# Kernel optimization log

Measured on AMD Instinct MI355X. Metric: run time of the kernel, lower is better.

## Reference

```python
import jax, jax.numpy as jnp
import numpy as np

NBITS = 3      # weight LSQ bits
PBITS = 8      # partial-sum LSQ bits
EPS = 1e-5


def round_ste(x):
    # straight-through round: identity gradient
    return x + jax.lax.stop_gradient(jnp.round(x) - x)


def lsq(x, alpha, nbits):
    # learned-step-size quantize/dequantize (symmetric signed)
    qn = -(2 ** (nbits - 1))
    qp = 2 ** (nbits - 1) - 1
    return round_ste(jnp.clip(x / alpha, qn, qp)) * alpha


def split_views(x):
    # x: [B,C,H,W] -> 9 shifted views of the 1-padded input, stacked [9,B,C,H,W]
    B, C, H, W = x.shape
    xp = jnp.pad(x, ((0, 0), (0, 0), (1, 1), (1, 1)))
    views = [xp[:, :, di:di + H, dj:dj + W] for dj in range(3) for di in range(3)]
    return jnp.stack(views, 0)


def split_conv3x3(x, w, wa, pa):
    # 3x3 conv emulated as 9 shifted 1x1 LSQ convs with quantized partial-sum accumulate
    # w: [9,O,C] per-tap 1x1 weights, wa: [9] weight step sizes, pa: [9] psum step sizes
    xs = split_views(x)                                      # [9,B,C,H,W]
    wq = jax.vmap(lambda wk, ak: lsq(wk, ak, NBITS))(w, wa)  # [9,O,C]
    ps = jnp.einsum('kbchw,koc->kbohw', xs, wq)              # 9 partial sums
    psq = lsq(ps, pa[:, None, None, None, None], PBITS)      # PartialSumLSQ each tap
    return psq.sum(0)                                        # accumulate -> [B,O,H,W]


def batchnorm(x, g, b):
    m = x.mean((0, 2, 3), keepdims=True)
    v = x.var((0, 2, 3), keepdims=True)
    return (x - m) / jnp.sqrt(v + EPS) * g[None, :, None, None] + b[None, :, None, None]


def setup_inputs() -> dict:
    key = jax.random.key(0)
    ks = jax.random.split(key, 8)
    B, C, O, H, W = 16, 128, 128, 56, 56
    x = jax.random.normal(ks[0], (B, C, H, W), jnp.float32)
    w1 = jax.random.normal(ks[1], (9, O, C), jnp.float32) * 0.05
    w2 = jax.random.normal(ks[2], (9, O, O), jnp.float32) * 0.05
    qp_w = 2 ** (NBITS - 1) - 1
    wa1 = 2.0 * jnp.mean(jnp.abs(w1), axis=(1, 2)) / np.sqrt(qp_w)
    wa2 = 2.0 * jnp.mean(jnp.abs(w2), axis=(1, 2)) / np.sqrt(qp_w)
    pa1 = jnp.full((9,), 0.05, jnp.float32)
    pa2 = jnp.full((9,), 0.05, jnp.float32)
    g1 = jnp.ones((O,), jnp.float32); b1 = jnp.zeros((O,), jnp.float32)
    g2 = jnp.ones((O,), jnp.float32); b2 = jnp.zeros((O,), jnp.float32)
    return {'x': x, 'w1': w1, 'wa1': wa1, 'pa1': pa1, 'g1': g1, 'b1': b1,
            'w2': w2, 'wa2': wa2, 'pa2': pa2, 'g2': g2, 'b2': b2}


def reference(x, w1, wa1, pa1, g1, b1, w2, wa2, pa2, g2, b2):
    identity = x
    out = split_conv3x3(x, w1, wa1, pa1)
    out = jax.nn.relu(batchnorm(out, g1, b1))
    out = split_conv3x3(out, w2, wa2, pa2)
    out = batchnorm(out, g2, b2)
    return jax.nn.relu(out + identity)
```

## Files before the change

kernel.cpp:

```cpp
#include <hip/hip_runtime.h>
#include <math.h>

typedef _Float16 f16;
typedef _Float16 half8 __attribute__((ext_vector_type(8)));
typedef float floatx16 __attribute__((ext_vector_type(16)));
typedef unsigned int u32;

#define HW_     3136
#define NPC     50176.0f
#define PB      3364
#define PPLANE  53824
#define ASTRIDE (2 * PPLANE * 16)

#define SW(c, px) (((px) + ((c) >> 2) + ((c) & 3) * 8) & 63)

typedef __attribute__((address_space(3))) u32 lds_u32;
typedef __attribute__((address_space(1))) u32 glb_u32;
__device__ __forceinline__ void async_copy16(const void* g, void* l) {
    __builtin_amdgcn_global_load_lds((const glb_u32*)g, (lds_u32*)l, 16, 0, 0);
}

__global__ __launch_bounds__(256) void prep_kernel(
        const float* __restrict__ w1, const float* __restrict__ wa1,
        const float* __restrict__ w2, const float* __restrict__ wa2,
        f16* __restrict__ W2a, f16* __restrict__ W2b) {
    const int idx = blockIdx.x * 256 + threadIdx.x;
    const float* w;
    const float* wa;
    f16* o;
    int m;
    if (idx < 18432) { w = w1; wa = wa1; o = W2a; m = idx; }
    else             { w = w2; wa = wa2; o = W2b; m = idx - 18432; }
    const int tap = m >> 11;
    const int r = m & 2047;
    const int k2 = r >> 7;
    const int oc = r & 127;
    const float a = wa[tap];
    const float* src = w + ((size_t)(tap * 128 + oc) * 128 + k2 * 8);
    half8 hv;
#pragma unroll
    for (int j = 0; j < 8; ++j)
        hv[j] = (f16)rintf(fminf(fmaxf(src[j] / a, -4.f), 3.f));
    *(half8*)(o + (size_t)m * 8) = hv;
}

__global__ __launch_bounds__(256) void pad_kernel(char* __restrict__ X2) {
    const int idx = blockIdx.x * 256 + threadIdx.x;
    const int k2 = idx / 3648;
    const int r = idx - k2 * 3648;
    const int b = r / 228;
    const int j = r - b * 228;
    int h, w;
    if (j < 58)        { h = 0;  w = j; }
    else if (j < 116)  { h = 57; w = j - 58; }
    else { const int k = j - 116; h = 1 + (k >> 1); w = (k & 1) * 57; }
    const size_t chunk = (size_t)k2 * PPLANE + (size_t)b * PB + h * 58 + w;
    float4 z = {0.f, 0.f, 0.f, 0.f};
    *(float4*)(X2 + chunk * 16) = z;
}

__global__ __launch_bounds__(256) void pack_kernel(
        const float* __restrict__ x, char* __restrict__ X2,
        float* __restrict__ stats) {
    const int t = threadIdx.x;
    const int blk = blockIdx.x;
    if (blk == 0 && t < 512) stats[t] = 0.f;
    const int b = blk / 49;
    const int p0 = (blk - b * 49) * 64;
    const int px = t & 63;
    const int cq = t >> 6;
    const int p = p0 + px;
    const int h = p / 56;
    const int w = p - h * 56;
    const size_t pp = (size_t)b * PB + (h + 1) * 58 + (w + 1);
    const float* xb = x + (size_t)b * 128 * HW_ + p;
#pragma unroll
    for (int s = 0; s < 4; ++s) {
        const int cg = s * 4 + cq;
        half8 hv, lv;
#pragma unroll
        for (int j = 0; j < 8; ++j) {
            const float v = xb[(size_t)(cg * 8 + j) * HW_];
            const f16 hh = (f16)v;
            hv[j] = hh;
            lv[j] = (f16)(v - (float)hh);
        }
        *(half8*)(X2 + ((size_t)cg * PPLANE + pp) * 16) = hv;
        *(half8*)(X2 + ((size_t)(cg + 16) * PPLANE + pp) * 16) = lv;
    }
}

__global__ __launch_bounds__(256, 2) void conv_kernel(
        const char* __restrict__ X2, const char* __restrict__ W2,
        const float* __restrict__ wav, const float* __restrict__ pav,
        float* __restrict__ cbuf, float* __restrict__ stats) {
    __shared__ f16 Bls[2][16384];
    __shared__ float red[512];
    const int t = threadIdx.x;
    const int lane = t & 63;
    const int wv = t >> 6;
    const int wm = wv & 1, wn = wv >> 1;
    const int tile = (blockIdx.x & 7) * 49 + (blockIdx.x >> 3);
    const int kh = lane >> 5;
    const int ln = lane & 31;

    int ppad[2];
#pragma unroll
    for (int mt = 0; mt < 2; ++mt) {
        const int gp = tile * 128 + wm * 64 + mt * 32 + ln;
        const int b = gp / HW_;
        const int p = gp - b * HW_;
        const int h = p / 56;
        const int w = p - h * 56;
        ppad[mt] = b * PB + (h + 1) * 58 + (w + 1);
    }
    int bdsoff[2];
#pragma unroll
    for (int nt = 0; nt < 2; ++nt)
        bdsoff[nt] = (kh * 128 + wn * 64 + nt * 32 + ln) * 16;
    const int sbase = wv * 8;

    floatx16 facc[2][2];
#pragma unroll
    for (int mt = 0; mt < 2; ++mt)
#pragma unroll
        for (int nt = 0; nt < 2; ++nt)
#pragma unroll
            for (int r = 0; r < 16; ++r) facc[mt][nt][r] = 0.f;

#pragma unroll
    for (int i = 0; i < 8; ++i)
        async_copy16(W2 + (((sbase + i) * 64 + lane) << 4),
                     (void*)&Bls[0][(sbase + i) * 512]);
    int aoff[2], aoffn[2];
#pragma unroll
    for (int mt = 0; mt < 2; ++mt) {
        aoff[mt] = ((ppad[mt] - 59) + kh * PPLANE) << 4;
        aoffn[mt] = aoff[mt];
    }
    half8 afr[2][8];
#pragma unroll
    for (int s0 = 0; s0 < 8; ++s0)
#pragma unroll
        for (int mt = 0; mt < 2; ++mt)
            afr[mt][s0] = *(const half8*)(X2 + aoff[mt] + s0 * ASTRIDE);
    __syncthreads();

    for (int tap = 0; tap < 9; ++tap) {
        const float pak = pav[tap];
        const float s1 = wav[tap] / pak;
        const char* bcur = (const char*)&Bls[tap & 1][0];
        if (tap < 8) {
            const char* wt = W2 + (tap + 1) * 32768;
            f16* bnxt = &Bls[(tap + 1) & 1][0];
#pragma unroll
            for (int i = 0; i < 8; ++i)
                async_copy16(wt + (((sbase + i) * 64 + lane) << 4),
                             (void*)&bnxt[(sbase + i) * 512]);
            const int dn = ((tap + 1) % 3 - 1) * 58 + ((tap + 1) / 3 - 1);
#pragma unroll
            for (int mt = 0; mt < 2; ++mt)
                aoffn[mt] = ((ppad[mt] + dn) + kh * PPLANE) << 4;
        }
        half8 bds[2][2];
#pragma unroll
        for (int nt = 0; nt < 2; ++nt)
#pragma unroll
            for (int sl = 0; sl < 2; ++sl)
                bds[nt][sl] = *(const half8*)(bcur + sl * 4096 + bdsoff[nt]);

        floatx16 acc[2][2];
#pragma unroll
        for (int mt = 0; mt < 2; ++mt)
#pragma unroll
            for (int nt = 0; nt < 2; ++nt)
#pragma unroll
                for (int r = 0; r < 16; ++r) acc[mt][nt][r] = 0.f;

#pragma unroll
        for (int s = 0; s < 16; ++s) {
#pragma unroll
            for (int nt = 0; nt < 2; ++nt)
#pragma unroll
                for (int mt = 0; mt < 2; ++mt)
                    acc[mt][nt] = __builtin_amdgcn_mfma_f32_32x32x16_f16(
                        afr[mt][s & 7], bds[nt][s & 1], acc[mt][nt], 0, 0, 0);
            if (s <= 13) {
                const int kf2 = (s + 2) & 7;
#pragma unroll
                for (int nt = 0; nt < 2; ++nt)
                    bds[nt][s & 1] =
                        *(const half8*)(bcur + kf2 * 4096 + bdsoff[nt]);
            }
            if (s < 8) {
#pragma unroll
                for (int mt = 0; mt < 2; ++mt)
                    afr[mt][s & 7] =
                        *(const half8*)(X2 + aoff[mt] + (s + 8) * ASTRIDE);
            } else if (tap < 8) {
#pragma unroll
                for (int mt = 0; mt < 2; ++mt)
                    afr[mt][s & 7] =
                        *(const half8*)(X2 + aoffn[mt] + (s - 8) * ASTRIDE);
            }
        }

#pragma unroll
        for (int mt = 0; mt < 2; ++mt)
#pragma unroll
            for (int nt = 0; nt < 2; ++nt)
#pragma unroll
                for (int r = 0; r < 16; ++r) {
                    const float q =
                        rintf(fminf(fmaxf(acc[mt][nt][r] * s1, -128.f), 127.f));
                    facc[mt][nt][r] = fmaf(q, pak, facc[mt][nt][r]);
                }
        aoff[0] = aoffn[0];
        aoff[1] = aoffn[1];
        __syncthreads();
    }

    const int gpb = tile * 128 + wm * 64;
    const int ocb = wn * 64 + ln;
#pragma unroll
    for (int mt = 0; mt < 2; ++mt)
#pragma unroll
        for (int r = 0; r < 16; ++r) {
            const int row = (r & 3) + 8 * (r >> 2) + 4 * kh;
            const int gp = gpb + mt * 32 + row;
            float* rp = cbuf + (size_t)gp * 128 + ocb;
            rp[0]  = facc[mt][0][r];
            rp[32] = facc[mt][1][r];
        }

    float sv[2], qv[2];
#pragma unroll
    for (int nt = 0; nt < 2; ++nt) {
        float s = 0.f, q = 0.f;
#pragma unroll
        for (int mt = 0; mt < 2; ++mt)
#pragma unroll
            for (int r = 0; r < 16; ++r) {
                const float v = facc[mt][nt][r];
                s += v;
                q = fmaf(v, v, q);
            }
        s += __shfl_xor(s, 32, 64);
        q += __shfl_xor(q, 32, 64);
        sv[nt] = s; qv[nt] = q;
    }
    if (lane < 32) {
#pragma unroll
        for (int nt = 0; nt < 2; ++nt) {
            const int oc = wn * 64 + nt * 32 + lane;
            red[oc * 2 + wm] = sv[nt];
            red[256 + oc * 2 + wm] = qv[nt];
        }
    }
    __syncthreads();
    if (t < 128) {
        atomicAdd(&stats[t],       red[2 * t] + red[2 * t + 1]);
        atomicAdd(&stats[128 + t], red[256 + 2 * t] + red[256 + 2 * t + 1]);
    }
}

__global__ __launch_bounds__(256) void bn_split_kernel(
        const float* __restrict__ cbuf, const float* __restrict__ stats,
        const float* __restrict__ g, const float* __restrict__ bb,
        char* __restrict__ X2) {
    __shared__ float xs[8192];
    __shared__ float scs[128], shs[128];
    const int t = threadIdx.x;
    if (t < 128) {
        const float m = stats[t] * (1.f / NPC);
        const float var = stats[128 + t] * (1.f / NPC) - m * m;
        const float inv = 1.f / sqrtf(var + 1e-5f);
        const float sc = g[t] * inv;
        scs[t] = sc;
        shs[t] = bb[t] - m * sc;
    }
    __syncthreads();
    const int blk = blockIdx.x;
#pragma unroll
    for (int i = 0; i < 8; ++i) {
        const int idx = i * 256 + t;
        const int px = idx >> 5;
        const int q = idx & 31;
        const float4 v = *(const float4*)&cbuf[(size_t)(blk * 64 + px) * 128 + q * 4];
        const float vv[4] = {v.x, v.y, v.z, v.w};
#pragma unroll
        for (int j = 0; j < 4; ++j) {
            const int c = q * 4 + j;
            xs[c * 64 + SW(c, px)] = fmaxf(fmaf(vv[j], scs[c], shs[c]), 0.f);
        }
    }
    __syncthreads();
    const int b = blk / 49;
    const int p0 = (blk - b * 49) * 64;
    const int px = t & 63;
    const int cq = t >> 6;
    const int p = p0 + px;
    const int h = p / 56;
    const int w = p - h * 56;
    const size_t pp = (size_t)b * PB + (h + 1) * 58 + (w + 1);
#pragma unroll
    for (int s = 0; s < 4; ++s) {
        const int cg = s * 4 + cq;
        half8 hv, lv;
#pragma unroll
        for (int j = 0; j < 8; ++j) {
            const int c = cg * 8 + j;
            const float v = xs[c * 64 + SW(c, px)];
            const f16 hh = (f16)v;
            hv[j] = hh;
            lv[j] = (f16)(v - (float)hh);
        }
        *(half8*)(X2 + ((size_t)cg * PPLANE + pp) * 16) = hv;
        *(half8*)(X2 + ((size_t)(cg + 16) * PPLANE + pp) * 16) = lv;
    }
}

__global__ __launch_bounds__(256) void final_kernel(
        const float* __restrict__ cbuf, const float* __restrict__ stats,
        const float* __restrict__ g, const float* __restrict__ bb,
        const float* __restrict__ resid, float* __restrict__ out) {
    __shared__ float xs[8192];
    __shared__ float scs[128], shs[128];
    const int t = threadIdx.x;
    if (t < 128) {
        const float m = stats[t] * (1.f / NPC);
        const float var = stats[128 + t] * (1.f / NPC) - m * m;
        const float inv = 1.f / sqrtf(var + 1e-5f);
        const float sc = g[t] * inv;
        scs[t] = sc;
        shs[t] = bb[t] - m * sc;
    }
    __syncthreads();
    const int blk = blockIdx.x;
#pragma unroll
    for (int i = 0; i < 8; ++i) {
        const int idx = i * 256 + t;
        const int px = idx >> 5;
        const int q = idx & 31;
        const float4 v = *(const float4*)&cbuf[(size_t)(blk * 64 + px) * 128 + q * 4];
        const float vv[4] = {v.x, v.y, v.z, v.w};
#pragma unroll
        for (int j = 0; j < 4; ++j) {
            const int c = q * 4 + j;
            xs[c * 64 + SW(c, px)] = fmaf(vv[j], scs[c], shs[c]);
        }
    }
    __syncthreads();
    const int b = blk / 49;
    const int p0 = (blk - b * 49) * 64;
    const int lane = t & 63, wq = t >> 6;
#pragma unroll
    for (int i = 0; i < 32; ++i) {
        const int c = i * 4 + wq;
        const float v = xs[c * 64 + SW(c, lane)];
        const size_t gi = (size_t)(b * 128 + c) * HW_ + p0 + lane;
        out[gi] = fmaxf(v + resid[gi], 0.f);
    }
}

extern "C" void kernel_launch(void* const* d_in, const int* in_sizes, int n_in,
                              void* d_out, int out_size, void* d_ws, size_t ws_size,
                              hipStream_t stream) {
    const float* x   = (const float*)d_in[0];
    const float* w1  = (const float*)d_in[1];
    const float* wa1 = (const float*)d_in[2];
    const float* pa1 = (const float*)d_in[3];
    const float* g1  = (const float*)d_in[4];
    const float* b1  = (const float*)d_in[5];
    const float* w2  = (const float*)d_in[6];
    const float* wa2 = (const float*)d_in[7];
    const float* pa2 = (const float*)d_in[8];
    const float* g2  = (const float*)d_in[9];
    const float* b2  = (const float*)d_in[10];
    float* out = (float*)d_out;

    char* ws = (char*)d_ws;
    char*  X2    = ws;
    float* cbuf  = (float*)(ws + 27557888);
    f16*   W2a   = (f16*)(ws + 53248000);
    f16*   W2b   = (f16*)(ws + 53542912);
    float* stats = (float*)(ws + 53837824);
    float* stats1 = stats;
    float* stats2 = stats + 256;

    hipLaunchKernelGGL(prep_kernel, dim3(144), dim3(256), 0, stream,
                       w1, wa1, w2, wa2, W2a, W2b);
    hipLaunchKernelGGL(pad_kernel, dim3(456), dim3(256), 0, stream, X2);
    hipLaunchKernelGGL(pack_kernel, dim3(784), dim3(256), 0, stream,
                       x, X2, stats);
    hipLaunchKernelGGL(conv_kernel, dim3(392), dim3(256), 0, stream,
                       X2, (const char*)W2a, wa1, pa1, cbuf, stats1);
    hipLaunchKernelGGL(bn_split_kernel, dim3(784), dim3(256), 0, stream,
                       cbuf, stats1, g1, b1, X2);
    hipLaunchKernelGGL(conv_kernel, dim3(392), dim3(256), 0, stream,
                       X2, (const char*)W2b, wa2, pa2, cbuf, stats2);
    hipLaunchKernelGGL(final_kernel, dim3(784), dim3(256), 0, stream,
                       cbuf, stats2, g2, b2, x, out);
}
```

Measured before the change: 211.0 us.

## Split conv tiles by output-channel half, drop LDS weight staging, fuse setup kernels

Result: slower. 380.6 us (+80.4%).

```diff
diff --git a/kernel.cpp b/kernel.cpp
--- a/kernel.cpp
+++ b/kernel.cpp
@@ -14,49 +14,43 @@
 
 #define SW(c, px) (((px) + ((c) >> 2) + ((c) & 3) * 8) & 63)
 
-typedef __attribute__((address_space(3))) u32 lds_u32;
-typedef __attribute__((address_space(1))) u32 glb_u32;
-__device__ __forceinline__ void async_copy16(const void* g, void* l) {
-    __builtin_amdgcn_global_load_lds((const glb_u32*)g, (lds_u32*)l, 16, 0, 0);
-}
-
-__global__ __launch_bounds__(256) void prep_kernel(
+__global__ __launch_bounds__(256) void setup_kernel(
         const float* __restrict__ w1, const float* __restrict__ wa1,
         const float* __restrict__ w2, const float* __restrict__ wa2,
-        f16* __restrict__ W2a, f16* __restrict__ W2b) {
+        f16* __restrict__ W2a, f16* __restrict__ W2b, char* __restrict__ X2) {
     const int idx = blockIdx.x * 256 + threadIdx.x;
-    const float* w;
-    const float* wa;
-    f16* o;
-    int m;
-    if (idx < 18432) { w = w1; wa = wa1; o = W2a; m = idx; }
-    else             { w = w2; wa = wa2; o = W2b; m = idx - 18432; }
-    const int tap = m >> 11;
-    const int r = m & 2047;
-    const int k2 = r >> 7;
-    const int oc = r & 127;
-    const float a = wa[tap];
-    const float* src = w + ((size_t)(tap * 128 + oc) * 128 + k2 * 8);
-    half8 hv;
-#pragma unroll
-    for (int j = 0; j < 8; ++j)
-        hv[j] = (f16)rintf(fminf(fmaxf(src[j] / a, -4.f), 3.f));
-    *(half8*)(o + (size_t)m * 8) = hv;
-}
-
-__global__ __launch_bounds__(256) void pad_kernel(char* __restrict__ X2) {
-    const int idx = blockIdx.x * 256 + threadIdx.x;
-    const int k2 = idx / 3648;
-    const int r = idx - k2 * 3648;
-    const int b = r / 228;
-    const int j = r - b * 228;
-    int h, w;
-    if (j < 58)        { h = 0;  w = j; }
-    else if (j < 116)  { h = 57; w = j - 58; }
-    else { const int k = j - 116; h = 1 + (k >> 1); w = (k & 1) * 57; }
-    const size_t chunk = (size_t)k2 * PPLANE + (size_t)b * PB + h * 58 + w;
-    float4 z = {0.f, 0.f, 0.f, 0.f};
-    *(float4*)(X2 + chunk * 16) = z;
+    if (idx < 36864) {
+        const float* w;
+        const float* wa;
+        f16* o;
+        int m;
+        if (idx < 18432) { w = w1; wa = wa1; o = W2a; m = idx; }
+        else             { w = w2; wa = wa2; o = W2b; m = idx - 18432; }
+        const int tap = m >> 11;
+        const int r = m & 2047;
+        const int k2 = r >> 7;
+        const int oc = r & 127;
+        const float a = wa[tap];
+        const float* src = w + ((size_t)(tap * 128 + oc) * 128 + k2 * 8);
+        half8 hv;
+#pragma unroll
+        for (int j = 0; j < 8; ++j)
+            hv[j] = (f16)rintf(fminf(fmaxf(src[j] / a, -4.f), 3.f));
+        *(half8*)(o + (size_t)m * 8) = hv;
+    } else {
+        const int m = idx - 36864;
+        const int k2 = m / 3648;
+        const int r = m - k2 * 3648;
+        const int b = r / 228;
+        const int j = r - b * 228;
+        int h, w;
+        if (j < 58)        { h = 0;  w = j; }
+        else if (j < 116)  { h = 57; w = j - 58; }
+        else { const int k = j - 116; h = 1 + (k >> 1); w = (k & 1) * 57; }
+        const size_t chunk = (size_t)k2 * PPLANE + (size_t)b * PB + h * 58 + w;
+        float4 z = {0.f, 0.f, 0.f, 0.f};
+        *(float4*)(X2 + chunk * 16) = z;
+    }
 }
 
 __global__ __launch_bounds__(256) void pack_kernel(
@@ -90,177 +84,123 @@
     }
 }
 
-__global__ __launch_bounds__(256, 2) void conv_kernel(
+__global__ __launch_bounds__(256, 3) void conv_kernel(
         const char* __restrict__ X2, const char* __restrict__ W2,
         const float* __restrict__ wav, const float* __restrict__ pav,
         float* __restrict__ cbuf, float* __restrict__ stats) {
-    __shared__ f16 Bls[2][16384];
-    __shared__ float red[512];
+    __shared__ float red[256];
     const int t = threadIdx.x;
     const int lane = t & 63;
     const int wv = t >> 6;
     const int wm = wv & 1, wn = wv >> 1;
-    const int tile = (blockIdx.x & 7) * 49 + (blockIdx.x >> 3);
-    const int kh = lane >> 5;
-    const int ln = lane & 31;
-
-    int ppad[2];
+    const int blk = (blockIdx.x & 7) * 98 + (blockIdx.x >> 3);
+    const int pxt = blk >> 1;
+    const int oh = blk & 1;
+    const int kh = lane >> 5, ln = lane & 31;
+    const int ocb = oh * 64 + wn * 32;
+    const int bv = (kh * 128 + ocb + ln) << 4;
+
+    int aoff[2];
 #pragma unroll
     for (int mt = 0; mt < 2; ++mt) {
-        const int gp = tile * 128 + wm * 64 + mt * 32 + ln;
+        const int gp = pxt * 128 + wm * 64 + mt * 32 + ln;
         const int b = gp / HW_;
         const int p = gp - b * HW_;
         const int h = p / 56;
         const int w = p - h * 56;
-        ppad[mt] = b * PB + (h + 1) * 58 + (w + 1);
-    }
-    int bdsoff[2];
-#pragma unroll
-    for (int nt = 0; nt < 2; ++nt)
-        bdsoff[nt] = (kh * 128 + wn * 64 + nt * 32 + ln) * 16;
-    const int sbase = wv * 8;
-
-    floatx16 facc[2][2];
+        aoff[mt] = ((b * PB + (h + 1) * 58 + (w + 1) - 59) + kh * PPLANE) << 4;
+    }
+
+    half8 bfr[8];
+#pragma unroll
+    for (int kf = 0; kf < 8; ++kf)
+        bfr[kf] = *(const half8*)(W2 + bv + kf * 4096);
+    half8 afr[2][4];
+#pragma unroll
+    for (int c = 0; c < 4; ++c)
+#pragma unroll
+        for (int mt = 0; mt < 2; ++mt)
+            afr[mt][c] = *(const half8*)(X2 + aoff[mt] + c * ASTRIDE);
+
+    floatx16 facc[2];
 #pragma unroll
     for (int mt = 0; mt < 2; ++mt)
 #pragma unroll
-        for (int nt = 0; nt < 2; ++nt)
-#pragma unroll
-            for (int r = 0; r < 16; ++r) facc[mt][nt][r] = 0.f;
-
-#pragma unroll
-    for (int i = 0; i < 8; ++i)
-        async_copy16(W2 + (((sbase + i) * 64 + lane) << 4),
-                     (void*)&Bls[0][(sbase + i) * 512]);
-    int aoff[2], aoffn[2];
-#pragma unroll
-    for (int mt = 0; mt < 2; ++mt) {
-        aoff[mt] = ((ppad[mt] - 59) + kh * PPLANE) << 4;
-        aoffn[mt] = aoff[mt];
-    }
-    half8 afr[2][8];
-#pragma unroll
-    for (int s0 = 0; s0 < 8; ++s0)
-#pragma unroll
-        for (int mt = 0; mt < 2; ++mt)
-            afr[mt][s0] = *(const half8*)(X2 + aoff[mt] + s0 * ASTRIDE);
-    __syncthreads();
+        for (int r = 0; r < 16; ++r) facc[mt][r] = 0.f;
 
     for (int tap = 0; tap < 9; ++tap) {
         const float pak = pav[tap];
         const float s1 = wav[tap] / pak;
-        const char* bcur = (const char*)&Bls[tap & 1][0];
-        if (tap < 8) {
-            const char* wt = W2 + (tap + 1) * 32768;
-            f16* bnxt = &Bls[(tap + 1) & 1][0];
-#pragma unroll
-            for (int i = 0; i < 8; ++i)
-                async_copy16(wt + (((sbase + i) * 64 + lane) << 4),
-                             (void*)&bnxt[(sbase + i) * 512]);
-            const int dn = ((tap + 1) % 3 - 1) * 58 + ((tap + 1) / 3 - 1);
-#pragma unroll
-            for (int mt = 0; mt < 2; ++mt)
-                aoffn[mt] = ((ppad[mt] + dn) + kh * PPLANE) << 4;
-        }
-        half8 bds[2][2];
-#pragma unroll
-        for (int nt = 0; nt < 2; ++nt)
-#pragma unroll
-            for (int sl = 0; sl < 2; ++sl)
-                bds[nt][sl] = *(const half8*)(bcur + sl * 4096 + bdsoff[nt]);
-
-        floatx16 acc[2][2];
+        const int dd = (((tap == 2) | (tap == 5)) ? -115 : 58) << 4;
+        const int aoffn0 = aoff[0] + dd;
+        const int aoffn1 = aoff[1] + dd;
+        const char* wnxt = W2 + (tap + 1) * 32768 + bv;
+
+        floatx16 acc[2];
 #pragma unroll
         for (int mt = 0; mt < 2; ++mt)
 #pragma unroll
-            for (int nt = 0; nt < 2; ++nt)
-#pragma unroll
-                for (int r = 0; r < 16; ++r) acc[mt][nt][r] = 0.f;
+            for (int r = 0; r < 16; ++r) acc[mt][r] = 0.f;
 
 #pragma unroll
         for (int s = 0; s < 16; ++s) {
-#pragma unroll
-            for (int nt = 0; nt < 2; ++nt)
-#pragma unroll
-                for (int mt = 0; mt < 2; ++mt)
-                    acc[mt][nt] = __builtin_amdgcn_mfma_f32_32x32x16_f16(
-                        afr[mt][s & 7], bds[nt][s & 1], acc[mt][nt], 0, 0, 0);
-            if (s <= 13) {
-                const int kf2 = (s + 2) & 7;
-#pragma unroll
-                for (int nt = 0; nt < 2; ++nt)
-                    bds[nt][s & 1] =
-                        *(const half8*)(bcur + kf2 * 4096 + bdsoff[nt]);
+            acc[0] = __builtin_amdgcn_mfma_f32_32x32x16_f16(
+                afr[0][s & 3], bfr[s & 7], acc[0], 0, 0, 0);
+            acc[1] = __builtin_amdgcn_mfma_f32_32x32x16_f16(
+                afr[1][s & 3], bfr[s & 7], acc[1], 0, 0, 0);
+            if (s < 12) {
+                afr[0][s & 3] = *(const half8*)(X2 + aoff[0] + (s + 4) * ASTRIDE);
+                afr[1][s & 3] = *(const half8*)(X2 + aoff[1] + (s + 4) * ASTRIDE);
+            } else if (tap < 8) {
+                afr[0][s & 3] = *(const half8*)(X2 + aoffn0 + (s - 12) * ASTRIDE);
+                afr[1][s & 3] = *(const half8*)(X2 + aoffn1 + (s - 12) * ASTRIDE);
             }
-            if (s < 8) {
-#pragma unroll
-                for (int mt = 0; mt < 2; ++mt)
-                    afr[mt][s & 7] =
-                        *(const half8*)(X2 + aoff[mt] + (s + 8) * ASTRIDE);
-            } else if (tap < 8) {
-#pragma unroll
-                for (int mt = 0; mt < 2; ++mt)
-                    afr[mt][s & 7] =
-                        *(const half8*)(X2 + aoffn[mt] + (s - 8) * ASTRIDE);
+            if (tap < 8 && s >= 8)
+                bfr[s - 8] = *(const half8*)(wnxt + (s - 8) * 4096);
+        }
+
+#pragma unroll
+        for (int mt = 0; mt < 2; ++mt)
+#pragma unroll
+            for (int r = 0; r < 16; ++r) {
+                const float q = rintf(
+                    __builtin_amdgcn_fmed3f(acc[mt][r] * s1, -128.f, 127.f));
+                facc[mt][r] = fmaf(q, pak, facc[mt][r]);
             }
-        }
-
-#pragma unroll
-        for (int mt = 0; mt < 2; ++mt)
-#pragma unroll
-            for (int nt = 0; nt < 2; ++nt)
-#pragma unroll
-                for (int r = 0; r < 16; ++r) {
-                    const float q =
-                        rintf(fminf(fmaxf(acc[mt][nt][r] * s1, -128.f), 127.f));
-                    facc[mt][nt][r] = fmaf(q, pak, facc[mt][nt][r]);
-                }
-        aoff[0] = aoffn[0];
-        aoff[1] = aoffn[1];
-        __syncthreads();
-    }
-
-    const int gpb = tile * 128 + wm * 64;
-    const int ocb = wn * 64 + ln;
+        aoff[0] = aoffn0;
+        aoff[1] = aoffn1;
+    }
+
+    const int gpb = pxt * 128 + wm * 64;
 #pragma unroll
     for (int mt = 0; mt < 2; ++mt)
 #pragma unroll
         for (int r = 0; r < 16; ++r) {
             const int row = (r & 3) + 8 * (r >> 2) + 4 * kh;
-            const int gp = gpb + mt * 32 + row;
-            float* rp = cbuf + (size_t)gp * 128 + ocb;
-            rp[0]  = facc[mt][0][r];
-            rp[32] = facc[mt][1][r];
-        }
-
-    float sv[2], qv[2];
-#pragma unroll
-    for (int nt = 0; nt < 2; ++nt) {
-        float s = 0.f, q = 0.f;
-#pragma unroll
-        for (int mt = 0; mt < 2; ++mt)
-#pragma unroll
-            for (int r = 0; r < 16; ++r) {
-                const float v = facc[mt][nt][r];
-                s += v;
-                q = fmaf(v, v, q);
-            }
-        s += __shfl_xor(s, 32, 64);
-        q += __shfl_xor(q, 32, 64);
-        sv[nt] = s; qv[nt] = q;
-    }
+            cbuf[(size_t)(gpb + mt * 32 + row) * 128 + ocb + ln] = facc[mt][r];
+        }
+
+    float s = 0.f, q = 0.f;
+#pragma unroll
+    for (int mt = 0; mt < 2; ++mt)
+#pragma unroll
+        for (int r = 0; r < 16; ++r) {
+            const float v = facc[mt][r];
+            s += v;
+            q = fmaf(v, v, q);
+        }
+    s += __shfl_xor(s, 32, 64);
+    q += __shfl_xor(q, 32, 64);
     if (lane < 32) {
-#pragma unroll
-        for (int nt = 0; nt < 2; ++nt) {
-            const int oc = wn * 64 + nt * 32 + lane;
-            red[oc * 2 + wm] = sv[nt];
-            red[256 + oc * 2 + wm] = qv[nt];
-        }
-    }
-    __syncthreads();
-    if (t < 128) {
-        atomicAdd(&stats[t],       red[2 * t] + red[2 * t + 1]);
-        atomicAdd(&stats[128 + t], red[256 + 2 * t] + red[256 + 2 * t + 1]);
+        const int ol = wn * 32 + lane;
+        red[ol * 2 + wm] = s;
+        red[128 + ol * 2 + wm] = q;
+    }
+    __syncthreads();
+    if (t < 64) {
+        atomicAdd(&stats[oh * 64 + t], red[2 * t] + red[2 * t + 1]);
+        atomicAdd(&stats[128 + oh * 64 + t],
+                  red[128 + 2 * t] + red[128 + 2 * t + 1]);
     }
 }
 
@@ -388,16 +328,15 @@
     float* stats1 = stats;
     float* stats2 = stats + 256;
 
-    hipLaunchKernelGGL(prep_kernel, dim3(144), dim3(256), 0, stream,
-                       w1, wa1, w2, wa2, W2a, W2b);
-    hipLaunchKernelGGL(pad_kernel, dim3(456), dim3(256), 0, stream, X2);
+    hipLaunchKernelGGL(setup_kernel, dim3(600), dim3(256), 0, stream,
+                       w1, wa1, w2, wa2, W2a, W2b, X2);
     hipLaunchKernelGGL(pack_kernel, dim3(784), dim3(256), 0, stream,
                        x, X2, stats);
-    hipLaunchKernelGGL(conv_kernel, dim3(392), dim3(256), 0, stream,
+    hipLaunchKernelGGL(conv_kernel, dim3(784), dim3(256), 0, stream,
                        X2, (const char*)W2a, wa1, pa1, cbuf, stats1);
     hipLaunchKernelGGL(bn_split_kernel, dim3(784), dim3(256), 0, stream,
                        cbuf, stats1, g1, b1, X2);
-    hipLaunchKernelGGL(conv_kernel, dim3(392), dim3(256), 0, stream,
+    hipLaunchKernelGGL(conv_kernel, dim3(784), dim3(256), 0, stream,
                        X2, (const char*)W2b, wa2, pa2, cbuf, stats2);
     hipLaunchKernelGGL(final_kernel, dim3(784), dim3(256), 0, stream,
                        cbuf, stats2, g2, b2, x, out);
```

## Halve conv pixel tile to 64, double grid, merge prep and pad kernels

Applied to the files above, without the earlier changes.

New measurement: 224.1 us. 1.06x slower.

```diff
diff --git a/kernel.cpp b/kernel.cpp
--- a/kernel.cpp
+++ b/kernel.cpp
@@ -20,43 +20,43 @@
     __builtin_amdgcn_global_load_lds((const glb_u32*)g, (lds_u32*)l, 16, 0, 0);
 }
 
-__global__ __launch_bounds__(256) void prep_kernel(
+__global__ __launch_bounds__(256) void setup_kernel(
         const float* __restrict__ w1, const float* __restrict__ wa1,
         const float* __restrict__ w2, const float* __restrict__ wa2,
-        f16* __restrict__ W2a, f16* __restrict__ W2b) {
+        f16* __restrict__ W2a, f16* __restrict__ W2b, char* __restrict__ X2) {
     const int idx = blockIdx.x * 256 + threadIdx.x;
-    const float* w;
-    const float* wa;
-    f16* o;
-    int m;
-    if (idx < 18432) { w = w1; wa = wa1; o = W2a; m = idx; }
-    else             { w = w2; wa = wa2; o = W2b; m = idx - 18432; }
-    const int tap = m >> 11;
-    const int r = m & 2047;
-    const int k2 = r >> 7;
-    const int oc = r & 127;
-    const float a = wa[tap];
-    const float* src = w + ((size_t)(tap * 128 + oc) * 128 + k2 * 8);
-    half8 hv;
-#pragma unroll
-    for (int j = 0; j < 8; ++j)
-        hv[j] = (f16)rintf(fminf(fmaxf(src[j] / a, -4.f), 3.f));
-    *(half8*)(o + (size_t)m * 8) = hv;
-}
-
-__global__ __launch_bounds__(256) void pad_kernel(char* __restrict__ X2) {
-    const int idx = blockIdx.x * 256 + threadIdx.x;
-    const int k2 = idx / 3648;
-    const int r = idx - k2 * 3648;
-    const int b = r / 228;
-    const int j = r - b * 228;
-    int h, w;
-    if (j < 58)        { h = 0;  w = j; }
-    else if (j < 116)  { h = 57; w = j - 58; }
-    else { const int k = j - 116; h = 1 + (k >> 1); w = (k & 1) * 57; }
-    const size_t chunk = (size_t)k2 * PPLANE + (size_t)b * PB + h * 58 + w;
-    float4 z = {0.f, 0.f, 0.f, 0.f};
-    *(float4*)(X2 + chunk * 16) = z;
+    if (idx < 36864) {
+        const float* w;
+        const float* wa;
+        f16* o;
+        int m;
+        if (idx < 18432) { w = w1; wa = wa1; o = W2a; m = idx; }
+        else             { w = w2; wa = wa2; o = W2b; m = idx - 18432; }
+        const int tap = m >> 11;
+        const int r = m & 2047;
+        const int k2 = r >> 7;
+        const int oc = r & 127;
+        const float a = wa[tap];
+        const float* src = w + ((size_t)(tap * 128 + oc) * 128 + k2 * 8);
+        half8 hv;
+#pragma unroll
+        for (int j = 0; j < 8; ++j)
+            hv[j] = (f16)rintf(fminf(fmaxf(src[j] / a, -4.f), 3.f));
+        *(half8*)(o + (size_t)m * 8) = hv;
+    } else {
+        const int m = idx - 36864;
+        const int k2 = m / 3648;
+        const int r = m - k2 * 3648;
+        const int b = r / 228;
+        const int j = r - b * 228;
+        int h, w;
+        if (j < 58)        { h = 0;  w = j; }
+        else if (j < 116)  { h = 57; w = j - 58; }
+        else { const int k = j - 116; h = 1 + (k >> 1); w = (k & 1) * 57; }
+        const size_t chunk = (size_t)k2 * PPLANE + (size_t)b * PB + h * 58 + w;
+        float4 z = {0.f, 0.f, 0.f, 0.f};
+        *(float4*)(X2 + chunk * 16) = z;
+    }
 }
 
 __global__ __launch_bounds__(256) void pack_kernel(
@@ -100,50 +100,39 @@
     const int lane = t & 63;
     const int wv = t >> 6;
     const int wm = wv & 1, wn = wv >> 1;
-    const int tile = (blockIdx.x & 7) * 49 + (blockIdx.x >> 3);
+    const int tile = (blockIdx.x & 7) * 98 + (blockIdx.x >> 3);
     const int kh = lane >> 5;
     const int ln = lane & 31;
 
-    int ppad[2];
-#pragma unroll
-    for (int mt = 0; mt < 2; ++mt) {
-        const int gp = tile * 128 + wm * 64 + mt * 32 + ln;
-        const int b = gp / HW_;
-        const int p = gp - b * HW_;
-        const int h = p / 56;
-        const int w = p - h * 56;
-        ppad[mt] = b * PB + (h + 1) * 58 + (w + 1);
-    }
+    const int gp = tile * 64 + wm * 32 + ln;
+    const int b = gp / HW_;
+    const int p = gp - b * HW_;
+    const int h = p / 56;
+    const int w = p - h * 56;
+    const int ppad = b * PB + (h + 1) * 58 + (w + 1);
+
     int bdsoff[2];
 #pragma unroll
     for (int nt = 0; nt < 2; ++nt)
         bdsoff[nt] = (kh * 128 + wn * 64 + nt * 32 + ln) * 16;
     const int sbase = wv * 8;
 
-    floatx16 facc[2][2];
-#pragma unroll
-    for (int mt = 0; mt < 2; ++mt)
-#pragma unroll
-        for (int nt = 0; nt < 2; ++nt)
-#pragma unroll
-            for (int r = 0; r < 16; ++r) facc[mt][nt][r] = 0.f;
+    floatx16 facc[2];
+#pragma unroll
+    for (int nt = 0; nt < 2; ++nt)
+#pragma unroll
+        for (int r = 0; r < 16; ++r) facc[nt][r] = 0.f;
 
 #pragma unroll
     for (int i = 0; i < 8; ++i)
         async_copy16(W2 + (((sbase + i) * 64 + lane) << 4),
                      (void*)&Bls[0][(sbase + i) * 512]);
-    int aoff[2], aoffn[2];
-#pragma unroll
-    for (int mt = 0; mt < 2; ++mt) {
-        aoff[mt] = ((ppad[mt] - 59) + kh * PPLANE) << 4;
-        aoffn[mt] = aoff[mt];
-    }
-    half8 afr[2][8];
+    int aoff = ((ppad - 59) + kh * PPLANE) << 4;
+    int aoffn = aoff;
+    half8 afr[8];
 #pragma unroll
     for (int s0 = 0; s0 < 8; ++s0)
-#pragma unroll
-        for (int mt = 0; mt < 2; ++mt)
-            afr[mt][s0] = *(const half8*)(X2 + aoff[mt] + s0 * ASTRIDE);
+        afr[s0] = *(const half8*)(X2 + aoff + s0 * ASTRIDE);
     __syncthreads();
 
     for (int tap = 0; tap < 9; ++tap) {
@@ -158,93 +147,72 @@
                 async_copy16(wt + (((sbase + i) * 64 + lane) << 4),
                              (void*)&bnxt[(sbase + i) * 512]);
             const int dn = ((tap + 1) % 3 - 1) * 58 + ((tap + 1) / 3 - 1);
-#pragma unroll
-            for (int mt = 0; mt < 2; ++mt)
-                aoffn[mt] = ((ppad[mt] + dn) + kh * PPLANE) << 4;
-        }
-        half8 bds[2][2];
+            aoffn = ((ppad + dn) + kh * PPLANE) << 4;
+        }
+        half8 bds[2][4];
 #pragma unroll
         for (int nt = 0; nt < 2; ++nt)
 #pragma unroll
-            for (int sl = 0; sl < 2; ++sl)
+            for (int sl = 0; sl < 4; ++sl)
                 bds[nt][sl] = *(const half8*)(bcur + sl * 4096 + bdsoff[nt]);
 
-        floatx16 acc[2][2];
-#pragma unroll
-        for (int mt = 0; mt < 2; ++mt)
-#pragma unroll
-            for (int nt = 0; nt < 2; ++nt)
-#pragma unroll
-                for (int r = 0; r < 16; ++r) acc[mt][nt][r] = 0.f;
+        floatx16 acc[2];
+#pragma unroll
+        for (int nt = 0; nt < 2; ++nt)
+#pragma unroll
+            for (int r = 0; r < 16; ++r) acc[nt][r] = 0.f;
 
 #pragma unroll
         for (int s = 0; s < 16; ++s) {
-#pragma unroll
-            for (int nt = 0; nt < 2; ++nt)
-#pragma unroll
-                for (int mt = 0; mt < 2; ++mt)
-                    acc[mt][nt] = __builtin_amdgcn_mfma_f32_32x32x16_f16(
-                        afr[mt][s & 7], bds[nt][s & 1], acc[mt][nt], 0, 0, 0);
-            if (s <= 13) {
-                const int kf2 = (s + 2) & 7;
+            acc[0] = __builtin_amdgcn_mfma_f32_32x32x16_f16(
+                afr[s & 7], bds[0][s & 3], acc[0], 0, 0, 0);
+            acc[1] = __builtin_amdgcn_mfma_f32_32x32x16_f16(
+                afr[s & 7], bds[1][s & 3], acc[1], 0, 0, 0);
+            if (s <= 11) {
+                const int kf4 = (s + 4) & 7;
 #pragma unroll
                 for (int nt = 0; nt < 2; ++nt)
-                    bds[nt][s & 1] =
-                        *(const half8*)(bcur + kf2 * 4096 + bdsoff[nt]);
+                    bds[nt][s & 3] =
+                        *(const half8*)(bcur + kf4 * 4096 + bdsoff[nt]);
             }
             if (s < 8) {
-#pragma unroll
-                for (int mt = 0; mt < 2; ++mt)
-                    afr[mt][s & 7] =
-                        *(const half8*)(X2 + aoff[mt] + (s + 8) * ASTRIDE);
+                afr[s & 7] = *(const half8*)(X2 + aoff + (s + 8) * ASTRIDE);
             } else if (tap < 8) {
-#pragma unroll
-                for (int mt = 0; mt < 2; ++mt)
-                    afr[mt][s & 7] =
-                        *(const half8*)(X2 + aoffn[mt] + (s - 8) * ASTRIDE);
+                afr[s & 7] = *(const half8*)(X2 + aoffn + (s - 8) * ASTRIDE);
             }
         }
 
 #pragma unroll
-        for (int mt = 0; mt < 2; ++mt)
-#pragma unroll
-            for (int nt = 0; nt < 2; ++nt)
-#pragma unroll
-                for (int r = 0; r < 16; ++r) {
-                    const float q =
-                        rintf(fminf(fmaxf(acc[mt][nt][r] * s1, -128.f), 127.f));
-                    facc[mt][nt][r] = fmaf(q, pak, facc[mt][nt][r]);
-                }
-        aoff[0] = aoffn[0];
-        aoff[1] = aoffn[1];
+        for (int nt = 0; nt < 2; ++nt)
+#pragma unroll
+            for (int r = 0; r < 16; ++r) {
+                const float q = rintf(
+                    __builtin_amdgcn_fmed3f(acc[nt][r] * s1, -128.f, 127.f));
+                facc[nt][r] = fmaf(q, pak, facc[nt][r]);
+            }
+        aoff = aoffn;
         __syncthreads();
     }
 
-    const int gpb = tile * 128 + wm * 64;
-    const int ocb = wn * 64 + ln;
-#pragma unroll
-    for (int mt = 0; mt < 2; ++mt)
-#pragma unroll
-        for (int r = 0; r < 16; ++r) {
-            const int row = (r & 3) + 8 * (r >> 2) + 4 * kh;
-            const int gp = gpb + mt * 32 + row;
-            float* rp = cbuf + (size_t)gp * 128 + ocb;
-            rp[0]  = facc[mt][0][r];
-            rp[32] = facc[mt][1][r];
-        }
+    const int gpb = tile * 64 + wm * 32;
+#pragma unroll
+    for (int r = 0; r < 16; ++r) {
+        const int row = (r & 3) + 8 * (r >> 2) + 4 * kh;
+        float* rp = cbuf + (size_t)(gpb + row) * 128 + wn * 64 + ln;
+        rp[0]  = facc[0][r];
+        rp[32] = facc[1][r];
+    }
 
     float sv[2], qv[2];
 #pragma unroll
     for (int nt = 0; nt < 2; ++nt) {
         float s = 0.f, q = 0.f;
 #pragma unroll
-        for (int mt = 0; mt < 2; ++mt)
-#pragma unroll
-            for (int r = 0; r < 16; ++r) {
-                const float v = facc[mt][nt][r];
-                s += v;
-                q = fmaf(v, v, q);
-            }
+        for (int r = 0; r < 16; ++r) {
+            const float v = facc[nt][r];
+            s += v;
+            q = fmaf(v, v, q);
+        }
         s += __shfl_xor(s, 32, 64);
         q += __shfl_xor(q, 32, 64);
         sv[nt] = s; qv[nt] = q;
@@ -388,16 +356,15 @@
     float* stats1 = stats;
     float* stats2 = stats + 256;
 
-    hipLaunchKernelGGL(prep_kernel, dim3(144), dim3(256), 0, stream,
-                       w1, wa1, w2, wa2, W2a, W2b);
-    hipLaunchKernelGGL(pad_kernel, dim3(456), dim3(256), 0, stream, X2);
+    hipLaunchKernelGGL(setup_kernel, dim3(600), dim3(256), 0, stream,
+                       w1, wa1, w2, wa2, W2a, W2b, X2);
     hipLaunchKernelGGL(pack_kernel, dim3(784), dim3(256), 0, stream,
                        x, X2, stats);
-    hipLaunchKernelGGL(conv_kernel, dim3(392), dim3(256), 0, stream,
+    hipLaunchKernelGGL(conv_kernel, dim3(784), dim3(256), 0, stream,
                        X2, (const char*)W2a, wa1, pa1, cbuf, stats1);
     hipLaunchKernelGGL(bn_split_kernel, dim3(784), dim3(256), 0, stream,
                        cbuf, stats1, g1, b1, X2);
-    hipLaunchKernelGGL(conv_kernel, dim3(392), dim3(256), 0, stream,
+    hipLaunchKernelGGL(conv_kernel, dim3(784), dim3(256), 0, stream,
                        X2, (const char*)W2b, wa2, pa2, cbuf, stats2);
     hipLaunchKernelGGL(final_kernel, dim3(784), dim3(256), 0, stream,
                        cbuf, stats2, g2, b2, x, out);
```
